# Kernel optimization log

Hardware: AMD Instinct MI355X
Metric: run time of the kernel (lower is better)

Reference implementation:

```python
import jax, jax.numpy as jnp
import numpy as np

N = 50000      # nodes
E = 800000     # edges (before self-loops)
F_IN = 64      # num_features
HID = 32       # hidden_channels
HEADS = 4
CLS = 3
NEG_SLOPE = 0.2  # PyG GATConv default


def setup_inputs() -> dict:
    key = jax.random.key(0)
    ks = jax.random.split(key, 12)
    s = 0.1
    return {
        "x": jax.random.normal(ks[0], (N, F_IN), jnp.float32),
        "W1": jax.random.normal(ks[1], (F_IN, HEADS * HID), jnp.float32) * s,
        "att_src1": jax.random.normal(ks[2], (HEADS, HID), jnp.float32) * s,
        "att_dst1": jax.random.normal(ks[3], (HEADS, HID), jnp.float32) * s,
        "b1": jnp.zeros((HEADS * HID,), jnp.float32),
        "W2": jax.random.normal(ks[4], (HEADS * HID, HID), jnp.float32) * s,
        "att_src2": jax.random.normal(ks[5], (1, HID), jnp.float32) * s,
        "att_dst2": jax.random.normal(ks[6], (1, HID), jnp.float32) * s,
        "b2": jnp.zeros((HID,), jnp.float32),
        "linW": jax.random.normal(ks[7], (HID, CLS), jnp.float32) * s,
        "linb": jnp.zeros((CLS,), jnp.float32),
        "edge_index": jax.random.randint(ks[8], (2, E), 0, N, dtype=jnp.int64),
    }


def _gat_conv(x, W, att_src, att_dst, bias, src, dst, heads):
    """PyG GATConv (eval mode, self-loops pre-added in src/dst)."""
    n = x.shape[0]
    h = (x @ W).reshape(n, heads, -1)                      # [N,H,C]
    a_src = jnp.sum(h * att_src, axis=-1)                  # [N,H]
    a_dst = jnp.sum(h * att_dst, axis=-1)                  # [N,H]
    e = jax.nn.leaky_relu(a_src[src] + a_dst[dst], NEG_SLOPE)  # [E,H]
    # segment softmax over destination node
    m = jax.ops.segment_max(e, dst, num_segments=n)
    p = jnp.exp(e - m[dst])
    denom = jax.ops.segment_sum(p, dst, num_segments=n)
    alpha = p / denom[dst]                                 # [E,H]
    msg = h[src] * alpha[:, :, None]                       # [E,H,C]
    out = jax.ops.segment_sum(msg, dst, num_segments=n)    # [N,H,C]
    return out.reshape(n, -1) + bias                       # concat heads


def reference(x, W1, att_src1, att_dst1, b1, W2, att_src2, att_dst2, b2, linW, linb, edge_index):
    n = x.shape[0]
    loop = jnp.arange(n, dtype=edge_index.dtype)
    src = jnp.concatenate([edge_index[0], loop])  # add self-loops (PyG default)
    dst = jnp.concatenate([edge_index[1], loop])
    h = _gat_conv(x, W1, att_src1, att_dst1, b1, src, dst, HEADS)
    h = jax.nn.elu(h)
    h = _gat_conv(h, W2, att_src2, att_dst2, b2, src, dst, 1)
    g = jnp.mean(h, axis=0, keepdims=True)        # batch is None path
    logits = g @ linW + linb                      # [1, CLS]
    return jax.nn.softmax(logits, axis=1)
```

## Files before the change

kernel.cpp:

```cpp
#include <hip/hip_runtime.h>
#include <hip/hip_fp16.h>
#include <math.h>

#define NEG_SLOPE 0.2f
#define CAP 64
#define SCB 2048

static __device__ __forceinline__ void atomAdd(float* a, float v) {
    unsafeAtomicAdd(a, v);
}

static __device__ __forceinline__ bool edges_are_i64(const int* __restrict__ ei) {
    return (ei[1] | ei[3] | ei[5] | ei[7]) == 0;
}
static __device__ __forceinline__ int ldsrc(const int* __restrict__ ei, int e, int E, bool i64) {
    return i64 ? ei[2 * e] : ei[e];
}
static __device__ __forceinline__ int lddst(const int* __restrict__ ei, int e, int E, bool i64) {
    return i64 ? ei[2 * (E + e)] : ei[E + e];
}

__global__ __launch_bounds__(256) void scatter_k(const int* __restrict__ ei,
                                                 int* __restrict__ deg,
                                                 int* __restrict__ col, int E, int N) {
    const int tid = threadIdx.x;
    const int grp = blockIdx.x & 7;
    const int bin = blockIdx.x >> 3;
    const int nb  = gridDim.x >> 3;
    const bool i64 = edges_are_i64(ei);
    const int ET = E + N;
    const int d0 = (int)((long long)grp * N / 8);
    const int d1 = (int)((long long)(grp + 1) * N / 8);
    for (int e = bin * 256 + tid; e < ET; e += nb * 256) {
        int s, d;
        if (e < E) { s = ldsrc(ei, e, E, i64); d = lddst(ei, e, E, i64); }
        else       { s = d = e - E; }
        if (d >= d0 && d < d1) {
            int pos = atomicAdd(&deg[d], 1);
            if (pos < CAP) col[d * CAP + pos] = s;
        }
    }
}

__global__ __launch_bounds__(256, 4) void gemm1_k(const float* __restrict__ x,
                                                  const float* __restrict__ W,
                                                  const float* __restrict__ aws,
                                                  const float* __restrict__ awd,
                                                  __half* __restrict__ h,
                                                  float* __restrict__ as_,
                                                  float* __restrict__ ad_, int N) {
    __shared__ float Ws[64 * 128];
    __shared__ float xs[32 * 64];
    const int tid = threadIdx.x;
    const int cg = tid & 31, rg = tid >> 5;
    const int r0 = blockIdx.x * 32;
#pragma unroll 1
    for (int i = tid; i < 8192; i += 256) Ws[i] = W[i];
    {
        const float* src = x + (size_t)r0 * 64;
        const int limit = (N - r0) * 64;
#pragma unroll 1
        for (int i = tid * 4; i < 2048; i += 1024) {
            float4 v = (i < limit) ? *(const float4*)(src + i) : make_float4(0, 0, 0, 0);
            *(float4*)(xs + i) = v;
        }
    }
    __syncthreads();

    float acc[4][4] = {};
#pragma unroll 2
    for (int k = 0; k < 64; k += 4) {
        float4 w0 = *(const float4*)(Ws + (k + 0) * 128 + cg * 4);
        float4 w1 = *(const float4*)(Ws + (k + 1) * 128 + cg * 4);
        float4 w2 = *(const float4*)(Ws + (k + 2) * 128 + cg * 4);
        float4 w3 = *(const float4*)(Ws + (k + 3) * 128 + cg * 4);
        float4 xv[4];
#pragma unroll
        for (int q = 0; q < 4; ++q) xv[q] = *(const float4*)(xs + (rg * 4 + q) * 64 + k);
#pragma unroll
        for (int q = 0; q < 4; ++q) {
            float4 xq = xv[q];
            acc[q][0] += xq.x * w0.x + xq.y * w1.x + xq.z * w2.x + xq.w * w3.x;
            acc[q][1] += xq.x * w0.y + xq.y * w1.y + xq.z * w2.y + xq.w * w3.y;
            acc[q][2] += xq.x * w0.z + xq.y * w1.z + xq.z * w2.z + xq.w * w3.z;
            acc[q][3] += xq.x * w0.w + xq.y * w1.w + xq.z * w2.w + xq.w * w3.w;
        }
    }

    const int jbase = cg * 4;
    const int head = cg >> 3;
    const float a0 = aws[jbase], a1 = aws[jbase + 1], a2 = aws[jbase + 2], a3 = aws[jbase + 3];
    const float d0 = awd[jbase], d1 = awd[jbase + 1], d2 = awd[jbase + 2], d3 = awd[jbase + 3];
    float ps[4], pd[4];
#pragma unroll
    for (int q = 0; q < 4; ++q) {
        ps[q] = acc[q][0] * a0 + acc[q][1] * a1 + acc[q][2] * a2 + acc[q][3] * a3;
        pd[q] = acc[q][0] * d0 + acc[q][1] * d1 + acc[q][2] * d2 + acc[q][3] * d3;
        int row = r0 + rg * 4 + q;
        if (row < N) {
            __half hv[4];
            hv[0] = __float2half(acc[q][0]); hv[1] = __float2half(acc[q][1]);
            hv[2] = __float2half(acc[q][2]); hv[3] = __float2half(acc[q][3]);
            *(uint2*)(h + (size_t)row * 128 + jbase) = *(uint2*)hv;
        }
    }
#pragma unroll
    for (int off = 4; off; off >>= 1) {
#pragma unroll
        for (int q = 0; q < 4; ++q) {
            ps[q] += __shfl_down(ps[q], off, 8);
            pd[q] += __shfl_down(pd[q], off, 8);
        }
    }
    if ((cg & 7) == 0) {
#pragma unroll
        for (int q = 0; q < 4; ++q) {
            int row = r0 + rg * 4 + q;
            if (row < N) { as_[row * 4 + head] = ps[q]; ad_[row * 4 + head] = pd[q]; }
        }
    }
}

__global__ __launch_bounds__(256, 4) void gemm2_k(const float* __restrict__ hact,
                                                  const float* __restrict__ W,
                                                  const float* __restrict__ aws,
                                                  const float* __restrict__ awd,
                                                  __half* __restrict__ h2,
                                                  float* __restrict__ as_,
                                                  float* __restrict__ ad_, int N) {
    __shared__ float Ws[128 * 32];
    __shared__ float xs[128 * 68];
    const int tid = threadIdx.x;
    const int cg = tid & 7, rg = tid >> 3;
    const int r0 = blockIdx.x * 128;
    for (int i = tid; i < 4096; i += 256) Ws[i] = W[i];

    float acc[4][4] = {};
#pragma unroll 1
    for (int p = 0; p < 2; ++p) {
        __syncthreads();
#pragma unroll 2
        for (int i = tid * 4; i < 8192; i += 1024) {
            int row = i >> 6, kk = i & 63;
            float4 v = (r0 + row < N)
                ? *(const float4*)(hact + (size_t)(r0 + row) * 128 + p * 64 + kk)
                : make_float4(0, 0, 0, 0);
            *(float4*)(xs + row * 68 + kk) = v;
        }
        __syncthreads();
#pragma unroll 2
        for (int k = 0; k < 64; k += 4) {
            float4 w0 = *(const float4*)(Ws + (p * 64 + k + 0) * 32 + cg * 4);
            float4 w1 = *(const float4*)(Ws + (p * 64 + k + 1) * 32 + cg * 4);
            float4 w2 = *(const float4*)(Ws + (p * 64 + k + 2) * 32 + cg * 4);
            float4 w3 = *(const float4*)(Ws + (p * 64 + k + 3) * 32 + cg * 4);
            float4 xv[4];
#pragma unroll
            for (int q = 0; q < 4; ++q) xv[q] = *(const float4*)(xs + (rg * 4 + q) * 68 + k);
#pragma unroll
            for (int q = 0; q < 4; ++q) {
                float4 xq = xv[q];
                acc[q][0] += xq.x * w0.x + xq.y * w1.x + xq.z * w2.x + xq.w * w3.x;
                acc[q][1] += xq.x * w0.y + xq.y * w1.y + xq.z * w2.y + xq.w * w3.y;
                acc[q][2] += xq.x * w0.z + xq.y * w1.z + xq.z * w2.z + xq.w * w3.z;
                acc[q][3] += xq.x * w0.w + xq.y * w1.w + xq.z * w2.w + xq.w * w3.w;
            }
        }
    }

    const int jbase = cg * 4;
    const float a0 = aws[jbase], a1 = aws[jbase + 1], a2 = aws[jbase + 2], a3 = aws[jbase + 3];
    const float d0 = awd[jbase], d1 = awd[jbase + 1], d2 = awd[jbase + 2], d3 = awd[jbase + 3];
    float ps[4], pd[4];
#pragma unroll
    for (int q = 0; q < 4; ++q) {
        ps[q] = acc[q][0] * a0 + acc[q][1] * a1 + acc[q][2] * a2 + acc[q][3] * a3;
        pd[q] = acc[q][0] * d0 + acc[q][1] * d1 + acc[q][2] * d2 + acc[q][3] * d3;
        int row = r0 + rg * 4 + q;
        if (row < N) {
            __half hv[4];
            hv[0] = __float2half(acc[q][0]); hv[1] = __float2half(acc[q][1]);
            hv[2] = __float2half(acc[q][2]); hv[3] = __float2half(acc[q][3]);
            *(uint2*)(h2 + (size_t)row * 32 + jbase) = *(uint2*)hv;
        }
    }
#pragma unroll
    for (int off = 4; off; off >>= 1) {
#pragma unroll
        for (int q = 0; q < 4; ++q) {
            ps[q] += __shfl_down(ps[q], off, 8);
            pd[q] += __shfl_down(pd[q], off, 8);
        }
    }
    if (cg == 0) {
#pragma unroll
        for (int q = 0; q < 4; ++q) {
            int row = r0 + rg * 4 + q;
            if (row < N) { as_[row] = ps[q]; ad_[row] = pd[q]; }
        }
    }
}

__global__ __launch_bounds__(256) void pull_agg1_k(const int* __restrict__ deg,
                                                   const int* __restrict__ col,
                                                   const float* __restrict__ asrc,
                                                   const float* __restrict__ adst,
                                                   const __half* __restrict__ h,
                                                   const float* __restrict__ b1,
                                                   float* __restrict__ hact, int N) {
    int wave = (blockIdx.x * 256 + threadIdx.x) >> 6;
    int lane = threadIdx.x & 63;
    if (wave >= N) return;
    const int d = wave;
    const int hd = lane >> 4;
    const float ad = adst[d * 4 + hd];
    const int* cl = col + d * CAP;
    int cnt = deg[d]; if (cnt > CAP) cnt = CAP;
    float acc0 = 0.0f, acc1 = 0.0f, den = 0.0f;
    int i = 0;
    for (; i + 8 <= cnt; i += 8) {
        int s[8]; float v[8]; __half2 g[8];
#pragma unroll
        for (int u = 0; u < 8; ++u) s[u] = cl[i + u];
#pragma unroll
        for (int u = 0; u < 8; ++u) v[u] = asrc[s[u] * 4 + hd] + ad;
#pragma unroll
        for (int u = 0; u < 8; ++u) g[u] = *(const __half2*)(h + (size_t)s[u] * 128 + lane * 2);
#pragma unroll
        for (int u = 0; u < 8; ++u) {
            float vv = v[u] > 0.0f ? v[u] : NEG_SLOPE * v[u];
            float p = __expf(vv);
            float2 gf = __half22float2(g[u]);
            den += p; acc0 += p * gf.x; acc1 += p * gf.y;
        }
    }
    for (; i < cnt; ++i) {
        int s = cl[i];
        float v = asrc[s * 4 + hd] + ad;
        v = v > 0.0f ? v : NEG_SLOPE * v;
        float p = __expf(v);
        float2 gf = __half22float2(*(const __half2*)(h + (size_t)s * 128 + lane * 2));
        den += p; acc0 += p * gf.x; acc1 += p * gf.y;
    }
    float inv = 1.0f / den;
    float o0 = acc0 * inv + b1[lane * 2];
    float o1 = acc1 * inv + b1[lane * 2 + 1];
    o0 = o0 > 0.0f ? o0 : expm1f(o0);
    o1 = o1 > 0.0f ? o1 : expm1f(o1);
    *(float2*)(hact + (size_t)d * 128 + lane * 2) = make_float2(o0, o1);
}

__global__ __launch_bounds__(256) void pull_agg2_k(const int* __restrict__ deg,
                                                   const int* __restrict__ col,
                                                   const float* __restrict__ asrc,
                                                   const float* __restrict__ adst,
                                                   const __half* __restrict__ h,
                                                   float* __restrict__ out, int N) {
    int grp = (blockIdx.x * 256 + threadIdx.x) >> 5;
    int lane = threadIdx.x & 31;
    if (grp >= N) return;
    const int d = grp;
    const float ad = adst[d];
    const int* cl = col + d * CAP;
    int cnt = deg[d]; if (cnt > CAP) cnt = CAP;
    float acc = 0.0f, den = 0.0f;
    int i = 0;
    for (; i + 8 <= cnt; i += 8) {
        int s[8]; float v[8]; __half g[8];
#pragma unroll
        for (int u = 0; u < 8; ++u) s[u] = cl[i + u];
#pragma unroll
        for (int u = 0; u < 8; ++u) v[u] = asrc[s[u]] + ad;
#pragma unroll
        for (int u = 0; u < 8; ++u) g[u] = h[(size_t)s[u] * 32 + lane];
#pragma unroll
        for (int u = 0; u < 8; ++u) {
            float vv = v[u] > 0.0f ? v[u] : NEG_SLOPE * v[u];
            float p = __expf(vv);
            den += p; acc += p * __half2float(g[u]);
        }
    }
    for (; i < cnt; ++i) {
        int s = cl[i];
        float v = asrc[s] + ad;
        v = v > 0.0f ? v : NEG_SLOPE * v;
        float p = __expf(v);
        den += p; acc += p * __half2float(h[(size_t)s * 32 + lane]);
    }
    out[(size_t)d * 32 + lane] = acc / den;
}

__global__ __launch_bounds__(256) void colmean_k(const float* __restrict__ out2,
                                                 float* __restrict__ gsum, int N) {
    __shared__ float lds[256];
    int tid = threadIdx.x;
    int c = tid % 32;
    int rg = tid / 32;
    float acc = 0.0f;
    for (int r = blockIdx.x * 8 + rg; r < N; r += gridDim.x * 8)
        acc += out2[(size_t)r * 32 + c];
    lds[tid] = acc;
    __syncthreads();
    if (tid < 32) {
        float s = 0.0f;
#pragma unroll
        for (int g = 0; g < 8; ++g) s += lds[g * 32 + tid];
        atomAdd(&gsum[tid], s);
    }
}

__global__ void final_k(const float* __restrict__ gsum, const float* __restrict__ b2w,
                        const float* __restrict__ linW, const float* __restrict__ linb,
                        float* __restrict__ out, int N) {
    if (threadIdx.x != 0 || blockIdx.x != 0) return;
    float g[32];
#pragma unroll
    for (int c = 0; c < 32; ++c) g[c] = gsum[c] / (float)N + b2w[c];
    float lo[3];
#pragma unroll
    for (int j = 0; j < 3; ++j) {
        float acc = linb[j];
#pragma unroll
        for (int c = 0; c < 32; ++c) acc += g[c] * linW[c * 3 + j];
        lo[j] = acc;
    }
    float mx = fmaxf(lo[0], fmaxf(lo[1], lo[2]));
    float ex[3], se = 0.0f;
#pragma unroll
    for (int j = 0; j < 3; ++j) { ex[j] = __expf(lo[j] - mx); se += ex[j]; }
#pragma unroll
    for (int j = 0; j < 3; ++j) out[j] = ex[j] / se;
}

extern "C" void kernel_launch(void* const* d_in, const int* in_sizes, int n_in,
                              void* d_out, int out_size, void* d_ws, size_t ws_size,
                              hipStream_t stream) {
    const float* x    = (const float*)d_in[0];
    const float* W1   = (const float*)d_in[1];
    const float* as1w = (const float*)d_in[2];
    const float* ad1w = (const float*)d_in[3];
    const float* b1   = (const float*)d_in[4];
    const float* W2   = (const float*)d_in[5];
    const float* as2w = (const float*)d_in[6];
    const float* ad2w = (const float*)d_in[7];
    const float* b2w  = (const float*)d_in[8];
    const float* linW = (const float*)d_in[9];
    const float* linb = (const float*)d_in[10];
    const int*   ei   = (const int*)d_in[11];

    const int N = in_sizes[0] / 64;
    const int E = in_sizes[11] / 2;

    float* ws = (float*)d_ws;
    __half* h1h  = (__half*)ws;
    float*  hact = ws + (size_t)N * 64;
    float* asrc1 = hact + (size_t)N * 128;
    float* adst1 = asrc1 + (size_t)N * 4;
    float* asrc2 = adst1 + (size_t)N * 4;
    float* adst2 = asrc2 + (size_t)N;
    float* gsum  = adst2 + (size_t)N;
    __half* h2h  = (__half*)ws;
    float*  out2 = ws + (size_t)N * 16;
    int* deg     = (int*)(gsum + 32);
    int* col     = deg + N;

    auto cdiv = [](int a, int b) { return (a + b - 1) / b; };

    hipMemsetAsync(deg, 0, (size_t)N * sizeof(int), stream);
    hipMemsetAsync(gsum, 0, 32 * sizeof(float), stream);

    scatter_k<<<SCB, 256, 0, stream>>>(ei, deg, col, E, N);

    gemm1_k<<<cdiv(N, 32), 256, 0, stream>>>(x, W1, as1w, ad1w, h1h, asrc1, adst1, N);
    pull_agg1_k<<<cdiv(N, 4), 256, 0, stream>>>(deg, col, asrc1, adst1, h1h, b1, hact, N);

    gemm2_k<<<cdiv(N, 128), 256, 0, stream>>>(hact, W2, as2w, ad2w, h2h, asrc2, adst2, N);
    pull_agg2_k<<<cdiv(N, 8), 256, 0, stream>>>(deg, col, asrc2, adst2, h2h, out2, N);

    colmean_k<<<256, 256, 0, stream>>>(out2, gsum, N);
    final_k<<<1, 64, 0, stream>>>(gsum, b2w, linW, linb, (float*)d_out, N);
}
```

Measured before the change: 248.3 us.

## Distribute edge-score computation across lanes and broadcast via shuffles in pull aggregation

```diff
diff --git a/kernel.cpp b/kernel.cpp
--- a/kernel.cpp
+++ b/kernel.cpp
@@ -213,35 +213,73 @@
     if (wave >= N) return;
     const int d = wave;
     const int hd = lane >> 4;
+    const int el = lane & 15;
     const float ad = adst[d * 4 + hd];
     const int* cl = col + d * CAP;
     int cnt = deg[d]; if (cnt > CAP) cnt = CAP;
     float acc0 = 0.0f, acc1 = 0.0f, den = 0.0f;
-    int i = 0;
-    for (; i + 8 <= cnt; i += 8) {
-        int s[8]; float v[8]; __half2 g[8];
-#pragma unroll
-        for (int u = 0; u < 8; ++u) s[u] = cl[i + u];
-#pragma unroll
-        for (int u = 0; u < 8; ++u) v[u] = asrc[s[u] * 4 + hd] + ad;
-#pragma unroll
-        for (int u = 0; u < 8; ++u) g[u] = *(const __half2*)(h + (size_t)s[u] * 128 + lane * 2);
-#pragma unroll
-        for (int u = 0; u < 8; ++u) {
-            float vv = v[u] > 0.0f ? v[u] : NEG_SLOPE * v[u];
-            float p = __expf(vv);
-            float2 gf = __half22float2(g[u]);
-            den += p; acc0 += p * gf.x; acc1 += p * gf.y;
-        }
-    }
-    for (; i < cnt; ++i) {
-        int s = cl[i];
+
+    const int full = cnt & ~15;
+    for (int i = 0; i < full; i += 16) {
+        int s = cl[i + el];
         float v = asrc[s * 4 + hd] + ad;
         v = v > 0.0f ? v : NEG_SLOPE * v;
         float p = __expf(v);
-        float2 gf = __half22float2(*(const __half2*)(h + (size_t)s * 128 + lane * 2));
-        den += p; acc0 += p * gf.x; acc1 += p * gf.y;
-    }
+        den += p;
+#pragma unroll
+        for (int hf = 0; hf < 2; ++hf) {
+            int su[8]; float pu[8]; __half2 g[8];
+#pragma unroll
+            for (int u = 0; u < 8; ++u) su[u] = __shfl(s, hf * 8 + u, 16);
+#pragma unroll
+            for (int u = 0; u < 8; ++u) g[u] = *(const __half2*)(h + (size_t)su[u] * 128 + lane * 2);
+#pragma unroll
+            for (int u = 0; u < 8; ++u) pu[u] = __shfl(p, hf * 8 + u, 16);
+#pragma unroll
+            for (int u = 0; u < 8; ++u) {
+                float2 gf = __half22float2(g[u]);
+                acc0 += pu[u] * gf.x; acc1 += pu[u] * gf.y;
+            }
+        }
+    }
+    const int rem = cnt - full;
+    if (rem) {
+        int s = 0; float p = 0.0f;
+        if (el < rem) {
+            s = cl[full + el];
+            float v = asrc[s * 4 + hd] + ad;
+            v = v > 0.0f ? v : NEG_SLOPE * v;
+            p = __expf(v);
+        }
+        den += p;
+        int u = 0;
+        if (rem >= 8) {
+            int su[8]; float pu[8]; __half2 g[8];
+#pragma unroll
+            for (int q = 0; q < 8; ++q) su[q] = __shfl(s, q, 16);
+#pragma unroll
+            for (int q = 0; q < 8; ++q) g[q] = *(const __half2*)(h + (size_t)su[q] * 128 + lane * 2);
+#pragma unroll
+            for (int q = 0; q < 8; ++q) pu[q] = __shfl(p, q, 16);
+#pragma unroll
+            for (int q = 0; q < 8; ++q) {
+                float2 gf = __half22float2(g[q]);
+                acc0 += pu[q] * gf.x; acc1 += pu[q] * gf.y;
+            }
+            u = 8;
+        }
+        for (; u < rem; ++u) {
+            int su = __shfl(s, u, 16);
+            float pu = __shfl(p, u, 16);
+            float2 gf = __half22float2(*(const __half2*)(h + (size_t)su * 128 + lane * 2));
+            acc0 += pu * gf.x; acc1 += pu * gf.y;
+        }
+    }
+    den += __shfl_xor(den, 1, 16);
+    den += __shfl_xor(den, 2, 16);
+    den += __shfl_xor(den, 4, 16);
+    den += __shfl_xor(den, 8, 16);
+
     float inv = 1.0f / den;
     float o0 = acc0 * inv + b1[lane * 2];
     float o1 = acc1 * inv + b1[lane * 2 + 1];
@@ -264,29 +302,60 @@
     const int* cl = col + d * CAP;
     int cnt = deg[d]; if (cnt > CAP) cnt = CAP;
     float acc = 0.0f, den = 0.0f;
-    int i = 0;
-    for (; i + 8 <= cnt; i += 8) {
-        int s[8]; float v[8]; __half g[8];
-#pragma unroll
-        for (int u = 0; u < 8; ++u) s[u] = cl[i + u];
-#pragma unroll
-        for (int u = 0; u < 8; ++u) v[u] = asrc[s[u]] + ad;
-#pragma unroll
-        for (int u = 0; u < 8; ++u) g[u] = h[(size_t)s[u] * 32 + lane];
-#pragma unroll
-        for (int u = 0; u < 8; ++u) {
-            float vv = v[u] > 0.0f ? v[u] : NEG_SLOPE * v[u];
-            float p = __expf(vv);
-            den += p; acc += p * __half2float(g[u]);
-        }
-    }
-    for (; i < cnt; ++i) {
-        int s = cl[i];
+
+    const int full = cnt & ~31;
+    for (int i = 0; i < full; i += 32) {
+        int s = cl[i + lane];
         float v = asrc[s] + ad;
         v = v > 0.0f ? v : NEG_SLOPE * v;
         float p = __expf(v);
-        den += p; acc += p * __half2float(h[(size_t)s * 32 + lane]);
-    }
+        den += p;
+#pragma unroll
+        for (int qb = 0; qb < 4; ++qb) {
+            int su[8]; float pu[8]; __half g[8];
+#pragma unroll
+            for (int u = 0; u < 8; ++u) su[u] = __shfl(s, qb * 8 + u, 32);
+#pragma unroll
+            for (int u = 0; u < 8; ++u) g[u] = h[(size_t)su[u] * 32 + lane];
+#pragma unroll
+            for (int u = 0; u < 8; ++u) pu[u] = __shfl(p, qb * 8 + u, 32);
+#pragma unroll
+            for (int u = 0; u < 8; ++u) acc += pu[u] * __half2float(g[u]);
+        }
+    }
+    const int rem = cnt - full;
+    if (rem) {
+        int s = 0; float p = 0.0f;
+        if (lane < rem) {
+            s = cl[full + lane];
+            float v = asrc[s] + ad;
+            v = v > 0.0f ? v : NEG_SLOPE * v;
+            p = __expf(v);
+        }
+        den += p;
+        int u = 0;
+        for (; u + 8 <= rem; u += 8) {
+            int su[8]; float pu[8]; __half g[8];
+#pragma unroll
+            for (int q = 0; q < 8; ++q) su[q] = __shfl(s, u + q, 32);
+#pragma unroll
+            for (int q = 0; q < 8; ++q) g[q] = h[(size_t)su[q] * 32 + lane];
+#pragma unroll
+            for (int q = 0; q < 8; ++q) pu[q] = __shfl(p, u + q, 32);
+#pragma unroll
+            for (int q = 0; q < 8; ++q) acc += pu[q] * __half2float(g[q]);
+        }
+        for (; u < rem; ++u) {
+            int su = __shfl(s, u, 32);
+            float pu = __shfl(p, u, 32);
+            acc += pu * __half2float(h[(size_t)su * 32 + lane]);
+        }
+    }
+    den += __shfl_xor(den, 1, 32);
+    den += __shfl_xor(den, 2, 32);
+    den += __shfl_xor(den, 4, 32);
+    den += __shfl_xor(den, 8, 32);
+    den += __shfl_xor(den, 16, 32);
     out[(size_t)d * 32 + lane] = acc / den;
 }
 
```

Result: no change. 246.7 us (-0.6%).

## Cooperative edge-weight compute with shuffles and fuse layer-2 aggregation with column mean

Applied to the files above, without the earlier changes.

```diff
diff --git a/kernel.cpp b/kernel.cpp
--- a/kernel.cpp
+++ b/kernel.cpp
@@ -24,13 +24,13 @@
                                                  int* __restrict__ deg,
                                                  int* __restrict__ col, int E, int N) {
     const int tid = threadIdx.x;
-    const int grp = blockIdx.x & 7;
-    const int bin = blockIdx.x >> 3;
-    const int nb  = gridDim.x >> 3;
+    const int grp = blockIdx.x & 3;
+    const int bin = blockIdx.x >> 2;
+    const int nb  = gridDim.x >> 2;
     const bool i64 = edges_are_i64(ei);
     const int ET = E + N;
-    const int d0 = (int)((long long)grp * N / 8);
-    const int d1 = (int)((long long)(grp + 1) * N / 8);
+    const int d0 = (int)((long long)grp * N / 4);
+    const int d1 = (int)((long long)(grp + 1) * N / 4);
     for (int e = bin * 256 + tid; e < ET; e += nb * 256) {
         int s, d;
         if (e < E) { s = ldsrc(ei, e, E, i64); d = lddst(ei, e, E, i64); }
@@ -213,35 +213,42 @@
     if (wave >= N) return;
     const int d = wave;
     const int hd = lane >> 4;
+    const int el = lane & 15;
     const float ad = adst[d * 4 + hd];
     const int* cl = col + d * CAP;
     int cnt = deg[d]; if (cnt > CAP) cnt = CAP;
     float acc0 = 0.0f, acc1 = 0.0f, den = 0.0f;
-    int i = 0;
-    for (; i + 8 <= cnt; i += 8) {
-        int s[8]; float v[8]; __half2 g[8];
-#pragma unroll
-        for (int u = 0; u < 8; ++u) s[u] = cl[i + u];
-#pragma unroll
-        for (int u = 0; u < 8; ++u) v[u] = asrc[s[u] * 4 + hd] + ad;
-#pragma unroll
-        for (int u = 0; u < 8; ++u) g[u] = *(const __half2*)(h + (size_t)s[u] * 128 + lane * 2);
-#pragma unroll
-        for (int u = 0; u < 8; ++u) {
-            float vv = v[u] > 0.0f ? v[u] : NEG_SLOPE * v[u];
-            float p = __expf(vv);
+
+    for (int i = 0; i < cnt; i += 16) {
+        const int r = cnt - i;
+        int s = 0; float p = 0.0f;
+        if (el < r) {
+            s = cl[i + el];
+            float v = asrc[s * 4 + hd] + ad;
+            v = v > 0.0f ? v : NEG_SLOPE * v;
+            p = __expf(v);
+        }
+        den += p;
+        int su[16];
+#pragma unroll
+        for (int u = 0; u < 16; ++u) su[u] = __shfl(s, u, 16);
+        __half2 g[16];
+#pragma unroll
+        for (int u = 0; u < 16; ++u) g[u] = *(const __half2*)(h + (size_t)su[u] * 128 + lane * 2);
+        float pu[16];
+#pragma unroll
+        for (int u = 0; u < 16; ++u) pu[u] = __shfl(p, u, 16);
+#pragma unroll
+        for (int u = 0; u < 16; ++u) {
             float2 gf = __half22float2(g[u]);
-            den += p; acc0 += p * gf.x; acc1 += p * gf.y;
-        }
-    }
-    for (; i < cnt; ++i) {
-        int s = cl[i];
-        float v = asrc[s * 4 + hd] + ad;
-        v = v > 0.0f ? v : NEG_SLOPE * v;
-        float p = __expf(v);
-        float2 gf = __half22float2(*(const __half2*)(h + (size_t)s * 128 + lane * 2));
-        den += p; acc0 += p * gf.x; acc1 += p * gf.y;
-    }
+            acc0 += pu[u] * gf.x; acc1 += pu[u] * gf.y;
+        }
+    }
+    den += __shfl_xor(den, 1, 16);
+    den += __shfl_xor(den, 2, 16);
+    den += __shfl_xor(den, 4, 16);
+    den += __shfl_xor(den, 8, 16);
+
     float inv = 1.0f / den;
     float o0 = acc0 * inv + b1[lane * 2];
     float o1 = acc1 * inv + b1[lane * 2 + 1];
@@ -255,57 +262,52 @@
                                                    const float* __restrict__ asrc,
                                                    const float* __restrict__ adst,
                                                    const __half* __restrict__ h,
-                                                   float* __restrict__ out, int N) {
-    int grp = (blockIdx.x * 256 + threadIdx.x) >> 5;
-    int lane = threadIdx.x & 31;
-    if (grp >= N) return;
-    const int d = grp;
-    const float ad = adst[d];
-    const int* cl = col + d * CAP;
-    int cnt = deg[d]; if (cnt > CAP) cnt = CAP;
-    float acc = 0.0f, den = 0.0f;
-    int i = 0;
-    for (; i + 8 <= cnt; i += 8) {
-        int s[8]; float v[8]; __half g[8];
-#pragma unroll
-        for (int u = 0; u < 8; ++u) s[u] = cl[i + u];
-#pragma unroll
-        for (int u = 0; u < 8; ++u) v[u] = asrc[s[u]] + ad;
-#pragma unroll
-        for (int u = 0; u < 8; ++u) g[u] = h[(size_t)s[u] * 32 + lane];
-#pragma unroll
-        for (int u = 0; u < 8; ++u) {
-            float vv = v[u] > 0.0f ? v[u] : NEG_SLOPE * v[u];
-            float p = __expf(vv);
-            den += p; acc += p * __half2float(g[u]);
-        }
-    }
-    for (; i < cnt; ++i) {
-        int s = cl[i];
-        float v = asrc[s] + ad;
-        v = v > 0.0f ? v : NEG_SLOPE * v;
-        float p = __expf(v);
-        den += p; acc += p * __half2float(h[(size_t)s * 32 + lane]);
-    }
-    out[(size_t)d * 32 + lane] = acc / den;
-}
-
-__global__ __launch_bounds__(256) void colmean_k(const float* __restrict__ out2,
-                                                 float* __restrict__ gsum, int N) {
+                                                   float* __restrict__ gsum, int N) {
+    const int lane = threadIdx.x & 31;
+    const int el = lane & 15;
+    const int gloc = threadIdx.x >> 5;
+    float csum = 0.0f;
+    for (int d = blockIdx.x * 8 + gloc; d < N; d += gridDim.x * 8) {
+        const float ad = adst[d];
+        const int* cl = col + d * CAP;
+        int cnt = deg[d]; if (cnt > CAP) cnt = CAP;
+        float acc = 0.0f, den = 0.0f;
+        for (int i = 0; i < cnt; i += 16) {
+            const int r = cnt - i;
+            int s = 0; float p = 0.0f;
+            if (el < r) {
+                s = cl[i + el];
+                float v = asrc[s] + ad;
+                v = v > 0.0f ? v : NEG_SLOPE * v;
+                p = __expf(v);
+            }
+            den += p;
+            int su[16];
+#pragma unroll
+            for (int u = 0; u < 16; ++u) su[u] = __shfl(s, u, 16);
+            __half gg[16];
+#pragma unroll
+            for (int u = 0; u < 16; ++u) gg[u] = h[(size_t)su[u] * 32 + lane];
+            float pu[16];
+#pragma unroll
+            for (int u = 0; u < 16; ++u) pu[u] = __shfl(p, u, 16);
+#pragma unroll
+            for (int u = 0; u < 16; ++u) acc += pu[u] * __half2float(gg[u]);
+        }
+        den += __shfl_xor(den, 1, 16);
+        den += __shfl_xor(den, 2, 16);
+        den += __shfl_xor(den, 4, 16);
+        den += __shfl_xor(den, 8, 16);
+        csum += acc / den;
+    }
     __shared__ float lds[256];
-    int tid = threadIdx.x;
-    int c = tid % 32;
-    int rg = tid / 32;
-    float acc = 0.0f;
-    for (int r = blockIdx.x * 8 + rg; r < N; r += gridDim.x * 8)
-        acc += out2[(size_t)r * 32 + c];
-    lds[tid] = acc;
+    lds[threadIdx.x] = csum;
     __syncthreads();
-    if (tid < 32) {
-        float s = 0.0f;
-#pragma unroll
-        for (int g = 0; g < 8; ++g) s += lds[g * 32 + tid];
-        atomAdd(&gsum[tid], s);
+    if (threadIdx.x < 32) {
+        float s2 = 0.0f;
+#pragma unroll
+        for (int g = 0; g < 8; ++g) s2 += lds[g * 32 + threadIdx.x];
+        atomAdd(&gsum[threadIdx.x], s2);
     }
 }
 
@@ -360,7 +362,6 @@
     float* adst2 = asrc2 + (size_t)N;
     float* gsum  = adst2 + (size_t)N;
     __half* h2h  = (__half*)ws;
-    float*  out2 = ws + (size_t)N * 16;
     int* deg     = (int*)(gsum + 32);
     int* col     = deg + N;
 
@@ -375,8 +376,7 @@
     pull_agg1_k<<<cdiv(N, 4), 256, 0, stream>>>(deg, col, asrc1, adst1, h1h, b1, hact, N);
 
     gemm2_k<<<cdiv(N, 128), 256, 0, stream>>>(hact, W2, as2w, ad2w, h2h, asrc2, adst2, N);
-    pull_agg2_k<<<cdiv(N, 8), 256, 0, stream>>>(deg, col, asrc2, adst2, h2h, out2, N);
-
-    colmean_k<<<256, 256, 0, stream>>>(out2, gsum, N);
+    pull_agg2_k<<<2048, 256, 0, stream>>>(deg, col, asrc2, adst2, h2h, gsum, N);
+
     final_k<<<1, 64, 0, stream>>>(gsum, b2w, linW, linb, (float*)d_out, N);
 }
```

Result: faster. 241.8 us (-2.6%).
